# Performance work log

Measured on AMD Instinct MI355X. Metric: run time of the kernel, lower is better.

## Reference

```python
import jax, jax.numpy as jnp
import numpy as np

B, S, D_MODEL, FILTER, K, MAX_FRAMES = 16, 512, 512, 512, 3, 2048


def _conv1d(x, w, b):
    # x: [B, C, L], w: [O, I, K], padding=1 -> same length
    y = jax.lax.conv_general_dilated(x, w, window_strides=(1,), padding=[(1, 1)],
                                     dimension_numbers=("NCH", "OIH", "NCH"))
    return y + b[None, :, None]


def _predictor(x, w1, b1, w2, b2, wl, bl):
    # x: [B, L, d] -> scalar track [B, L]
    h = x.transpose(0, 2, 1)                      # [B, d, L]
    h = jax.nn.relu(_conv1d(h, w1, b1))
    h = jax.nn.relu(_conv1d(h, w2, b2))
    h = h.transpose(0, 2, 1)                      # [B, L, filter]
    return (jnp.einsum("blf,f->bl", h, wl[:, 0]) + bl[0])


def _expand_hidden(H, D, max_T):
    # Length regulator: cumsum + searchsorted gather (vectorized repeat_interleave).
    D = jnp.maximum(D, 0).astype(jnp.int32)
    csum = jnp.cumsum(D, axis=1)                  # [B, S]
    t = jnp.arange(max_T, dtype=jnp.int32)        # [T]
    # idx[b, t] = # of cumsum entries <= t  == source token index for frame t
    idx = jax.vmap(lambda c: jnp.searchsorted(c, t, side="right"))(csum)  # [B, T]
    total = csum[:, -1]                           # [B]
    valid = t[None, :] < jnp.minimum(total, max_T)[:, None]               # [B, T]
    idx_safe = jnp.minimum(idx, S - 1)
    He = jnp.take_along_axis(H, idx_safe[:, :, None], axis=1)             # [B, T, d]
    return jnp.where(valid[:, :, None], He, jnp.zeros((), He.dtype))


def setup_inputs() -> dict:
    key = jax.random.key(0)
    ks = jax.random.split(key, 24)
    def w(k, shape, scale=0.05):
        return jax.random.normal(k, shape, dtype=jnp.float32) * scale
    inp = {
        "H": jax.random.normal(ks[0], (B, S, D_MODEL), dtype=jnp.float32),
        "D_gt": jax.random.randint(ks[1], (B, S), 0, 12, dtype=jnp.int32),
        "P_gt": jax.random.normal(ks[2], (B, MAX_FRAMES), dtype=jnp.float32),
        "E_gt": jax.random.normal(ks[3], (B, MAX_FRAMES), dtype=jnp.float32),
    }
    for i, p in enumerate(["dp", "pp", "ep"]):
        kk = jax.random.split(ks[4 + i], 3)
        inp[p + "_w1"] = w(kk[0], (FILTER, D_MODEL, K))
        inp[p + "_b1"] = jnp.zeros((FILTER,), jnp.float32)
        inp[p + "_w2"] = w(kk[1], (FILTER, FILTER, K))
        inp[p + "_b2"] = jnp.zeros((FILTER,), jnp.float32)
        inp[p + "_wl"] = w(kk[2], (FILTER, 1))
        inp[p + "_bl"] = jnp.zeros((1,), jnp.float32)
    inp["pitch_w"] = w(ks[8], (D_MODEL,))
    inp["pitch_b"] = jnp.zeros((D_MODEL,), jnp.float32)
    inp["energy_w"] = w(ks[9], (D_MODEL,))
    inp["energy_b"] = jnp.zeros((D_MODEL,), jnp.float32)
    return inp


def reference(H, D_gt, P_gt, E_gt,
              dp_w1, dp_b1, dp_w2, dp_b2, dp_wl, dp_bl,
              pp_w1, pp_b1, pp_w2, pp_b2, pp_wl, pp_bl,
              ep_w1, ep_b1, ep_w2, ep_b2, ep_wl, ep_bl,
              pitch_w, pitch_b, energy_w, energy_b):
    # Training path (is_inference=False): D = D_gt, P = P_gt, E = E_gt.
    D_pred = _predictor(H, dp_w1, dp_b1, dp_w2, dp_b2, dp_wl, dp_bl)     # [B, S]
    H_exp = _expand_hidden(H, D_gt, MAX_FRAMES)                           # [B, T, d]
    P_pred = _predictor(H_exp, pp_w1, pp_b1, pp_w2, pp_b2, pp_wl, pp_bl)  # [B, T]
    E_pred = _predictor(H_exp, ep_w1, ep_b1, ep_w2, ep_b2, ep_wl, ep_bl)  # [B, T]
    P_proj = P_gt[:, :, None] * pitch_w[None, None, :] + pitch_b          # Linear(1,d)
    E_proj = E_gt[:, :, None] * energy_w[None, None, :] + energy_b
    H_adapted = H_exp + P_proj + E_proj
    return (H_adapted, D_pred, P_pred, E_pred)
```

## Files before the change

kernel.cpp:

```cpp
#include <hip/hip_runtime.h>

#define B_ 16
#define S_ 512
#define C_ 512
#define T_ 2048

typedef __attribute__((ext_vector_type(8))) short short8;
typedef __attribute__((ext_vector_type(4))) float floatx4;

__device__ __forceinline__ unsigned short f2bf(float x) {
    union { float f; unsigned u; } c; c.f = x;
    unsigned r = (c.u + 0x7fffu + ((c.u >> 16) & 1u)) >> 16;
    return (unsigned short)r;
}

__device__ __forceinline__ void gld_lds16(void* l, const void* g) {
    __builtin_amdgcn_global_load_lds(
        (const __attribute__((address_space(1))) void*)g,
        (__attribute__((address_space(3))) void*)l, 16, 0, 0);
}

__global__ void prep_kernel(const float* __restrict__ w0, const float* __restrict__ w1,
                            const float* __restrict__ w2, const float* __restrict__ w3,
                            const float* __restrict__ w4, const float* __restrict__ w5,
                            unsigned short* __restrict__ wpack,
                            const float* __restrict__ H, unsigned short* __restrict__ Hbf,
                            unsigned short* __restrict__ zrow,
                            const int* __restrict__ Dgt, int* __restrict__ ridx,
                            float* __restrict__ Dp, float* __restrict__ Pp, float* __restrict__ Ep,
                            const float* __restrict__ dbl, const float* __restrict__ pbl,
                            const float* __restrict__ ebl) {
    __shared__ int cs[S_];
    __shared__ int ps[256];
    int blk = blockIdx.x;
    int tid = threadIdx.x;
    if (blk < 6144) {
        int which = blk >> 10;
        const float* w = which == 0 ? w0 : which == 1 ? w1 : which == 2 ? w2
                       : which == 3 ? w3 : which == 4 ? w4 : w5;
        unsigned short* wp = wpack + (long)which * 786432;
        int i = (blk & 1023) * 256 + tid;
        const float* s = w + (long)i * 3;
        wp[i]          = f2bf(s[0]);
        wp[i + 262144] = f2bf(s[1]);
        wp[i + 524288] = f2bf(s[2]);
    } else if (blk < 10240) {
        int i = (blk - 6144) * 256 + tid;
        float4 v = *(const float4*)(H + (long)i * 4);
        ushort4 o;
        o.x = f2bf(v.x); o.y = f2bf(v.y); o.z = f2bf(v.z); o.w = f2bf(v.w);
        *(ushort4*)(Hbf + (long)i * 4) = o;
    } else if (blk < 10242) {
        zrow[(blk - 10240) * 256 + tid] = 0;
    } else if (blk < 10258) {
        int b = blk - 10242;
        int t2 = tid * 2;
        int d0 = Dgt[b * S_ + t2], d1 = Dgt[b * S_ + t2 + 1];
        int a0 = d0 < 0 ? 0 : d0, a1 = d1 < 0 ? 0 : d1;
        ps[tid] = a0 + a1;
        __syncthreads();
        for (int off = 1; off < 256; off <<= 1) {
            int v = (tid >= off) ? ps[tid - off] : 0;
            __syncthreads();
            ps[tid] += v;
            __syncthreads();
        }
        int incl = ps[tid];
        cs[t2] = incl - a1;
        cs[t2 + 1] = incl;
        __syncthreads();
        int total = cs[S_ - 1];
        int limit = total < T_ ? total : T_;
        for (int t = tid; t < T_; t += 256) {
            int lo = 0, hi = S_;
            while (lo < hi) { int mid = (lo + hi) >> 1; if (cs[mid] <= t) lo = mid + 1; else hi = mid; }
            if (lo > S_ - 1) lo = S_ - 1;
            ridx[b * T_ + t] = (t < limit) ? lo : -1;
        }
    } else {
        int i = (blk - 10258) * 256 + tid;
        if (i < 8192) Dp[i] = dbl[0];
        else if (i < 40960) Pp[i - 8192] = pbl[0];
        else Ep[i - 40960] = ebl[0];
    }
}

struct ConvJob {
    const unsigned short* X;
    const int* ridx;
    int Lshift;
    int Bshift;
    const unsigned short* wp;
    const float* bias;
    const float* wl;
    void* dst;
    int nxshift;
};

__global__ __launch_bounds__(256, 3) void mega_kernel(
    ConvJob j0, ConvJob j1, ConvJob j2, int e0, int e1, int e2, int mode, int aoff,
    const unsigned short* __restrict__ zrow,
    const float* __restrict__ H, const int* __restrict__ aridx,
    const float* __restrict__ Pgt, const float* __restrict__ Egt,
    const float* __restrict__ pw, const float* __restrict__ pb,
    const float* __restrict__ ew, const float* __restrict__ eb,
    float* __restrict__ aout)
{
    __shared__ unsigned short Wt[3 * 128 * 32];
    __shared__ unsigned short Xt[136 * 32 + 4096];
    const int bx = blockIdx.x;
    const int tid = threadIdx.x;

    if (bx >= e2) {
        int ab = bx - e2 + aoff;
#pragma unroll
        for (int it = 0; it < 8; ++it) {
            int i = ab * 256 + tid + it * 524288;
            int f4 = i & 127;
            int p  = i >> 7;
            int b  = p >> 11;
            int r  = aridx[p];
            float pg = Pgt[p], eg = Egt[p];
            int f = f4 << 2;
            float4 pwv = *(const float4*)(pw + f);
            float4 pbv = *(const float4*)(pb + f);
            float4 ewv = *(const float4*)(ew + f);
            float4 ebv = *(const float4*)(eb + f);
            float4 h = make_float4(0.f, 0.f, 0.f, 0.f);
            if (r >= 0) h = *(const float4*)(H + ((long)b * S_ + r) * C_ + f);
            float4 o;
            o.x = h.x + pg * pwv.x + pbv.x + eg * ewv.x + ebv.x;
            o.y = h.y + pg * pwv.y + pbv.y + eg * ewv.y + ebv.y;
            o.z = h.z + pg * pwv.z + pbv.z + eg * ewv.z + ebv.z;
            o.w = h.w + pg * pwv.w + pbv.w + eg * ewv.w + ebv.w;
            *(float4*)(aout + (long)p * C_ + f) = o;
        }
        return;
    }

    ConvJob j;
    int local;
    if (bx < e0)      { j = j0; local = bx; }
    else if (bx < e1) { j = j1; local = bx - e0; }
    else              { j = j2; local = bx - e1; }
    const int m0 = (local >> j.nxshift) * 128;
    const int n0 = (local & ((1 << j.nxshift) - 1)) * 128;
    const int L = 1 << j.Lshift;
    const int b = n0 >> j.Lshift;
    const int t0 = n0 & (L - 1);

    floatx4 acc[4][4];
#pragma unroll
    for (int i = 0; i < 4; ++i)
#pragma unroll
        for (int jj = 0; jj < 4; ++jj) acc[i][jj] = (floatx4){0.f, 0.f, 0.f, 0.f};

    const unsigned short* wptr[6];
#pragma unroll
    for (int q = 0; q < 6; ++q) {
        int idx = tid + q * 256;
        int tap = idx >> 9, rem = idx & 511;
        int row = rem >> 2;
        int sw = (rem & 3) ^ ((row >> 1) & 3);
        wptr[q] = j.wp + (long)tap * (C_ * C_) + (long)(m0 + row) * C_ + sw * 8;
    }
    auto xrow = [&](int rho) -> const unsigned short* {
        int t = t0 - 1 + rho;
        if (t < 0 || t >= L) return zrow;
        int r = j.ridx ? j.ridx[(b << j.Lshift) + t] : t;
        if (r < 0) return zrow;
        return j.X + ((long)(b << j.Bshift) + r) * C_;
    };
    const int xs = tid & 3;
    const int rho0 = tid >> 2, rho1 = 64 + (tid >> 2), rho2 = 128 + (tid >> 2);
    const unsigned short* xptr0 = xrow(rho0) + (xs ^ ((rho0 >> 1) & 3)) * 8;
    const unsigned short* xptr1 = xrow(rho1) + (xs ^ ((rho1 >> 1) & 3)) * 8;
    const unsigned short* xptr2 = (tid < 8) ? (xrow(rho2) + (xs ^ ((rho2 >> 1) & 3)) * 8) : zrow;

    char* wbase = (char*)Wt + (tid >> 6) * 1024;
    char* xbase = (char*)Xt + (tid >> 6) * 1024;

    const int lane = tid & 63;
    const int q = lane >> 4, lr = lane & 15;
    const int wm = (tid >> 6) & 1, wn = tid >> 7;
    const int qsW = (q ^ ((lr >> 1) & 3)) * 8;
    int qsX[3];
#pragma unroll
    for (int tap = 0; tap < 3; ++tap)
        qsX[tap] = (q ^ (((lr + tap) >> 1) & 3)) * 8;

    for (int c0 = 0; c0 < C_; c0 += 32) {
        __syncthreads();
#pragma unroll
        for (int qq = 0; qq < 6; ++qq)
            gld_lds16(wbase + qq * 4096, wptr[qq] + c0);
        gld_lds16(xbase, xptr0 + c0);
        gld_lds16(xbase + 4096, xptr1 + c0);
        if (tid < 8)
            gld_lds16((char*)Xt + 8192, xptr2 + c0);
        __syncthreads();
#pragma unroll
        for (int tap = 0; tap < 3; ++tap) {
            const unsigned short* Wl = Wt + ((tap * 128) + wm * 64 + lr) * 32 + qsW;
            const unsigned short* Xl = Xt + (wn * 64 + lr + tap) * 32 + qsX[tap];
            short8 a[4], bf[4];
#pragma unroll
            for (int i = 0; i < 4; ++i) {
                a[i]  = *(const short8*)(Wl + i * 16 * 32);
                bf[i] = *(const short8*)(Xl + i * 16 * 32);
            }
#pragma unroll
            for (int i = 0; i < 4; ++i)
#pragma unroll
                for (int jj = 0; jj < 4; ++jj)
                    acc[i][jj] = __builtin_amdgcn_mfma_f32_16x16x32_bf16(
                        a[i], bf[jj], acc[i][jj], 0, 0, 0);
        }
    }

    const int fbase = m0 + wm * 64 + q * 4;
    const int pbase = n0 + wn * 64 + lr;
    if (mode == 0) {
        unsigned short* dst = (unsigned short*)j.dst;
#pragma unroll
        for (int i = 0; i < 4; ++i) {
            int f = fbase + i * 16;
            float4 bv = *(const float4*)(j.bias + f);
#pragma unroll
            for (int jj = 0; jj < 4; ++jj) {
                int p = pbase + jj * 16;
                ushort4 o;
                o.x = f2bf(fmaxf(acc[i][jj][0] + bv.x, 0.f));
                o.y = f2bf(fmaxf(acc[i][jj][1] + bv.y, 0.f));
                o.z = f2bf(fmaxf(acc[i][jj][2] + bv.z, 0.f));
                o.w = f2bf(fmaxf(acc[i][jj][3] + bv.w, 0.f));
                *(ushort4*)(dst + (long)p * C_ + f) = o;
            }
        }
    } else {
        float* dst = (float*)j.dst;
#pragma unroll
        for (int jj = 0; jj < 4; ++jj) {
            float s = 0.f;
#pragma unroll
            for (int i = 0; i < 4; ++i) {
                int f = fbase + i * 16;
                float4 bv = *(const float4*)(j.bias + f);
                float4 wv = *(const float4*)(j.wl + f);
                s += fmaxf(acc[i][jj][0] + bv.x, 0.f) * wv.x;
                s += fmaxf(acc[i][jj][1] + bv.y, 0.f) * wv.y;
                s += fmaxf(acc[i][jj][2] + bv.z, 0.f) * wv.z;
                s += fmaxf(acc[i][jj][3] + bv.w, 0.f) * wv.w;
            }
            s += __shfl_xor(s, 16, 64);
            s += __shfl_xor(s, 32, 64);
            if (lane < 16) atomicAdd(dst + pbase + jj * 16, s);
        }
    }
}

extern "C" void kernel_launch(void* const* d_in, const int* in_sizes, int n_in,
                              void* d_out, int out_size, void* d_ws, size_t ws_size,
                              hipStream_t stream) {
    const float* H    = (const float*)d_in[0];
    const int*   Dgt  = (const int*)d_in[1];
    const float* Pgt  = (const float*)d_in[2];
    const float* Egt  = (const float*)d_in[3];
    const float* dp_w1 = (const float*)d_in[4];
    const float* dp_b1 = (const float*)d_in[5];
    const float* dp_w2 = (const float*)d_in[6];
    const float* dp_b2 = (const float*)d_in[7];
    const float* dp_wl = (const float*)d_in[8];
    const float* dp_bl = (const float*)d_in[9];
    const float* pp_w1 = (const float*)d_in[10];
    const float* pp_b1 = (const float*)d_in[11];
    const float* pp_w2 = (const float*)d_in[12];
    const float* pp_b2 = (const float*)d_in[13];
    const float* pp_wl = (const float*)d_in[14];
    const float* pp_bl = (const float*)d_in[15];
    const float* ep_w1 = (const float*)d_in[16];
    const float* ep_b1 = (const float*)d_in[17];
    const float* ep_w2 = (const float*)d_in[18];
    const float* ep_b2 = (const float*)d_in[19];
    const float* ep_wl = (const float*)d_in[20];
    const float* ep_bl = (const float*)d_in[21];
    const float* pitch_w  = (const float*)d_in[22];
    const float* pitch_b  = (const float*)d_in[23];
    const float* energy_w = (const float*)d_in[24];
    const float* energy_b = (const float*)d_in[25];

    float* out     = (float*)d_out;
    float* H_adapt = out;
    float* D_pred  = out + 16777216;
    float* P_pred  = out + 16785408;
    float* E_pred  = out + 16818176;

    const bool par = ws_size >= 94000000ull;

    char* ws = (char*)d_ws;
    size_t off = 0;
    unsigned short* wpack = (unsigned short*)(ws + off); off += 6UL * 786432UL * 2UL;
    unsigned short* Hbf   = (unsigned short*)(ws + off); off += 4194304UL * 2UL;
    unsigned short* h1a   = (unsigned short*)(ws + off); off += 16777216UL * 2UL;
    unsigned short* h1b   = par ? (unsigned short*)(ws + off) : h1a;
    if (par) off += 16777216UL * 2UL;
    unsigned short* h1dp  = (unsigned short*)(ws + off); off += 4194304UL * 2UL;
    unsigned short* zrow  = (unsigned short*)(ws + off); off += 512UL * 2UL;
    off = (off + 255) & ~(size_t)255;
    int* ridx_exp = (int*)(ws + off); off += (size_t)B_ * T_ * 4;

    hipLaunchKernelGGL(prep_kernel, dim3(10546), dim3(256), 0, stream,
                       dp_w1, dp_w2, pp_w1, pp_w2, ep_w1, ep_w2, wpack, H, Hbf, zrow,
                       Dgt, ridx_exp, D_pred, P_pred, E_pred, dp_bl, pp_bl, ep_bl);

    ConvJob j_pp1 = { Hbf,  ridx_exp, 11,  9, wpack + 2UL * 786432, pp_b1, nullptr, h1a,    8 };
    ConvJob j_ep1 = { Hbf,  ridx_exp, 11,  9, wpack + 4UL * 786432, ep_b1, nullptr, h1b,    8 };
    ConvJob j_dp1 = { Hbf,  nullptr,   9,  9, wpack + 0UL * 786432, dp_b1, nullptr, h1dp,   6 };
    ConvJob j_pp2 = { h1a,  nullptr,  11, 11, wpack + 3UL * 786432, pp_b2, pp_wl,  P_pred, 8 };
    ConvJob j_ep2 = { h1b,  nullptr,  11, 11, wpack + 5UL * 786432, ep_b2, ep_wl,  E_pred, 8 };
    ConvJob j_dp2 = { h1dp, nullptr,   9,  9, wpack + 1UL * 786432, dp_b2, dp_wl,  D_pred, 6 };

    if (par) {
        hipLaunchKernelGGL(mega_kernel, dim3(2304 + 1024), dim3(256), 0, stream,
                           j_pp1, j_ep1, j_dp1, 1024, 2048, 2304, 0, 0, zrow,
                           H, ridx_exp, Pgt, Egt, pitch_w, pitch_b, energy_w, energy_b, H_adapt);
        hipLaunchKernelGGL(mega_kernel, dim3(2304 + 1024), dim3(256), 0, stream,
                           j_pp2, j_ep2, j_dp2, 1024, 2048, 2304, 1, 1024, zrow,
                           H, ridx_exp, Pgt, Egt, pitch_w, pitch_b, energy_w, energy_b, H_adapt);
    } else {
        hipLaunchKernelGGL(mega_kernel, dim3(1280 + 2048), dim3(256), 0, stream,
                           j_pp1, j_dp1, j_dp1, 1024, 1280, 1280, 0, 0, zrow,
                           H, ridx_exp, Pgt, Egt, pitch_w, pitch_b, energy_w, energy_b, H_adapt);
        hipLaunchKernelGGL(mega_kernel, dim3(1280), dim3(256), 0, stream,
                           j_pp2, j_dp2, j_dp2, 1024, 1280, 1280, 1, 0, zrow,
                           H, ridx_exp, Pgt, Egt, pitch_w, pitch_b, energy_w, energy_b, H_adapt);
        hipLaunchKernelGGL(mega_kernel, dim3(1024), dim3(256), 0, stream,
                           j_ep1, j_ep1, j_ep1, 1024, 1024, 1024, 0, 0, zrow,
                           H, ridx_exp, Pgt, Egt, pitch_w, pitch_b, energy_w, energy_b, H_adapt);
        hipLaunchKernelGGL(mega_kernel, dim3(1024), dim3(256), 0, stream,
                           j_ep2, j_ep2, j_ep2, 1024, 1024, 1024, 1, 0, zrow,
                           H, ridx_exp, Pgt, Egt, pitch_w, pitch_b, energy_w, energy_b, H_adapt);
    }
}
```

Baseline: 359.4 us.

## Use 256x256 tiles with 8 waves and double-buffered LDS pipelined conv GEMM

The conv GEMM tile grows from 128x128 to 256x256, with 512-thread blocks, a 64-wide K chunk and 130KB of dynamic LDS. Weight and activation tiles are double-buffered, and the global-to-LDS loads for the next tap or chunk are interleaved between MFMA phases, using s_setprio and explicit vmcnt waits. The goal is to raise arithmetic intensity and hide load latency behind MFMA work. In exchange the grid is much smaller (576 conv blocks on about 256 CUs), so tail effects may appear, and the large LDS footprint limits occupancy to one block per CU.

New measurement: 515.1 us. 43.3% more time.

```diff
diff --git a/kernel.cpp b/kernel.cpp
--- a/kernel.cpp
+++ b/kernel.cpp
@@ -97,7 +97,53 @@
     int nxshift;
 };
 
-__global__ __launch_bounds__(256, 3) void mega_kernel(
+template <int TAP, typename F0, typename F1, typename F2, typename F3>
+__device__ __forceinline__ void kt_body(
+    floatx4 (&acc)[8][4],
+    const unsigned short* __restrict__ Wb_, const unsigned short* __restrict__ Xb_,
+    int wm, int wn, int q, int lr, F0 s0, F1 s1, F2 s2, F3 s3)
+{
+    short8 bfr[4][2];
+#pragma unroll
+    for (int jj = 0; jj < 4; ++jj) {
+        const int xr = wn * 64 + jj * 16 + lr + TAP;
+        const unsigned short* xp = Xb_ + xr * 64;
+        const int sX = xr & 7;
+        bfr[jj][0] = *(const short8*)(xp + ((q ^ sX) * 8));
+        bfr[jj][1] = *(const short8*)(xp + (((4 + q) ^ sX) * 8));
+    }
+#pragma unroll
+    for (int ph = 0; ph < 4; ++ph) {
+        const int wr = wm * 128 + ph * 32 + lr;
+        const unsigned short* ap0 = Wb_ + wr * 64;
+        const unsigned short* ap1 = ap0 + 1024;
+        const int sA = lr & 7;
+        short8 a00 = *(const short8*)(ap0 + ((q ^ sA) * 8));
+        short8 a01 = *(const short8*)(ap0 + (((4 + q) ^ sA) * 8));
+        short8 a10 = *(const short8*)(ap1 + ((q ^ sA) * 8));
+        short8 a11 = *(const short8*)(ap1 + (((4 + q) ^ sA) * 8));
+        if (ph == 0) s0(); else if (ph == 1) s1(); else if (ph == 2) s2(); else s3();
+        __builtin_amdgcn_s_setprio(1);
+#pragma unroll
+        for (int jj = 0; jj < 4; ++jj) {
+            acc[ph*2][jj]   = __builtin_amdgcn_mfma_f32_16x16x32_bf16(a00, bfr[jj][0], acc[ph*2][jj],   0, 0, 0);
+            acc[ph*2][jj]   = __builtin_amdgcn_mfma_f32_16x16x32_bf16(a01, bfr[jj][1], acc[ph*2][jj],   0, 0, 0);
+            acc[ph*2+1][jj] = __builtin_amdgcn_mfma_f32_16x16x32_bf16(a10, bfr[jj][0], acc[ph*2+1][jj], 0, 0, 0);
+            acc[ph*2+1][jj] = __builtin_amdgcn_mfma_f32_16x16x32_bf16(a11, bfr[jj][1], acc[ph*2+1][jj], 0, 0, 0);
+        }
+        __builtin_amdgcn_s_setprio(0);
+        __builtin_amdgcn_s_barrier();
+    }
+}
+
+#define VMWAIT(n) do { \
+    asm volatile("s_waitcnt vmcnt(" #n ")" ::: "memory"); \
+    __builtin_amdgcn_sched_barrier(0); \
+    __builtin_amdgcn_s_barrier(); \
+    __builtin_amdgcn_sched_barrier(0); \
+} while (0)
+
+__global__ __launch_bounds__(512, 2) void mega_kernel(
     ConvJob j0, ConvJob j1, ConvJob j2, int e0, int e1, int e2, int mode, int aoff,
     const unsigned short* __restrict__ zrow,
     const float* __restrict__ H, const int* __restrict__ aridx,
@@ -106,8 +152,7 @@
     const float* __restrict__ ew, const float* __restrict__ eb,
     float* __restrict__ aout)
 {
-    __shared__ unsigned short Wt[3 * 128 * 32];
-    __shared__ unsigned short Xt[136 * 32 + 4096];
+    extern __shared__ unsigned short lds[];
     const int bx = blockIdx.x;
     const int tid = threadIdx.x;
 
@@ -115,7 +160,7 @@
         int ab = bx - e2 + aoff;
 #pragma unroll
         for (int it = 0; it < 8; ++it) {
-            int i = ab * 256 + tid + it * 524288;
+            int i = ab * 512 + tid + it * 524288;
             int f4 = i & 127;
             int p  = i >> 7;
             int b  = p >> 11;
@@ -143,87 +188,100 @@
     if (bx < e0)      { j = j0; local = bx; }
     else if (bx < e1) { j = j1; local = bx - e0; }
     else              { j = j2; local = bx - e1; }
-    const int m0 = (local >> j.nxshift) * 128;
-    const int n0 = (local & ((1 << j.nxshift) - 1)) * 128;
+    const int m0 = (local >> j.nxshift) * 256;
+    const int n0 = (local & ((1 << j.nxshift) - 1)) * 256;
     const int L = 1 << j.Lshift;
     const int b = n0 >> j.Lshift;
     const int t0 = n0 & (L - 1);
 
-    floatx4 acc[4][4];
-#pragma unroll
-    for (int i = 0; i < 4; ++i)
+    unsigned short* WtS = lds;
+    unsigned short* XtS = lds + 32768;
+    char* WtB = (char*)WtS;
+    char* XtB = (char*)XtS;
+
+    const int w = tid >> 6, l = tid & 63;
+    const int q = l >> 4, lr = l & 15;
+    const int wm = w & 1, wn = w >> 1;
+
+    floatx4 acc[8][4];
+#pragma unroll
+    for (int i = 0; i < 8; ++i)
 #pragma unroll
         for (int jj = 0; jj < 4; ++jj) acc[i][jj] = (floatx4){0.f, 0.f, 0.f, 0.f};
 
-    const unsigned short* wptr[6];
-#pragma unroll
-    for (int q = 0; q < 6; ++q) {
-        int idx = tid + q * 256;
-        int tap = idx >> 9, rem = idx & 511;
-        int row = rem >> 2;
-        int sw = (rem & 3) ^ ((row >> 1) & 3);
-        wptr[q] = j.wp + (long)tap * (C_ * C_) + (long)(m0 + row) * C_ + sw * 8;
-    }
-    auto xrow = [&](int rho) -> const unsigned short* {
-        int t = t0 - 1 + rho;
+    const int swz = ((l & 7) ^ ((l >> 3) & 7)) * 8;
+    auto xrowp = [&](int r) -> const unsigned short* {
+        int t = t0 - 1 + r;
         if (t < 0 || t >= L) return zrow;
-        int r = j.ridx ? j.ridx[(b << j.Lshift) + t] : t;
-        if (r < 0) return zrow;
-        return j.X + ((long)(b << j.Bshift) + r) * C_;
+        int rr = j.ridx ? j.ridx[(b << j.Lshift) + t] : t;
+        if (rr < 0) return zrow;
+        return j.X + ((long)(b << j.Bshift) + rr) * C_;
     };
-    const int xs = tid & 3;
-    const int rho0 = tid >> 2, rho1 = 64 + (tid >> 2), rho2 = 128 + (tid >> 2);
-    const unsigned short* xptr0 = xrow(rho0) + (xs ^ ((rho0 >> 1) & 3)) * 8;
-    const unsigned short* xptr1 = xrow(rho1) + (xs ^ ((rho1 >> 1) & 3)) * 8;
-    const unsigned short* xptr2 = (tid < 8) ? (xrow(rho2) + (xs ^ ((rho2 >> 1) & 3)) * 8) : zrow;
-
-    char* wbase = (char*)Wt + (tid >> 6) * 1024;
-    char* xbase = (char*)Xt + (tid >> 6) * 1024;
-
-    const int lane = tid & 63;
-    const int q = lane >> 4, lr = lane & 15;
-    const int wm = (tid >> 6) & 1, wn = tid >> 7;
-    const int qsW = (q ^ ((lr >> 1) & 3)) * 8;
-    int qsX[3];
-#pragma unroll
-    for (int tap = 0; tap < 3; ++tap)
-        qsX[tap] = (q ^ (((lr + tap) >> 1) & 3)) * 8;
-
-    for (int c0 = 0; c0 < C_; c0 += 32) {
-        __syncthreads();
-#pragma unroll
-        for (int qq = 0; qq < 6; ++qq)
-            gld_lds16(wbase + qq * 4096, wptr[qq] + c0);
-        gld_lds16(xbase, xptr0 + c0);
-        gld_lds16(xbase + 4096, xptr1 + c0);
-        if (tid < 8)
-            gld_lds16((char*)Xt + 8192, xptr2 + c0);
-        __syncthreads();
-#pragma unroll
-        for (int tap = 0; tap < 3; ++tap) {
-            const unsigned short* Wl = Wt + ((tap * 128) + wm * 64 + lr) * 32 + qsW;
-            const unsigned short* Xl = Xt + (wn * 64 + lr + tap) * 32 + qsX[tap];
-            short8 a[4], bf[4];
-#pragma unroll
-            for (int i = 0; i < 4; ++i) {
-                a[i]  = *(const short8*)(Wl + i * 16 * 32);
-                bf[i] = *(const short8*)(Xl + i * 16 * 32);
-            }
-#pragma unroll
-            for (int i = 0; i < 4; ++i)
-#pragma unroll
-                for (int jj = 0; jj < 4; ++jj)
-                    acc[i][jj] = __builtin_amdgcn_mfma_f32_16x16x32_bf16(
-                        a[i], bf[jj], acc[i][jj], 0, 0, 0);
-        }
-    }
-
-    const int fbase = m0 + wm * 64 + q * 4;
+    const unsigned short* wsrc[4];
+    const unsigned short* xsrc[4];
+#pragma unroll
+    for (int qq = 0; qq < 4; ++qq) {
+        int row = qq * 64 + w * 8 + (l >> 3);
+        wsrc[qq] = j.wp + (long)(m0 + row) * C_ + swz;
+        xsrc[qq] = xrowp(row) + swz;
+    }
+    const int ch_e = w * 2 + (l & 1);
+    const int row_e = 256 + (ch_e >> 3);
+    const unsigned short* xsrcE = xrowp(row_e) + (((ch_e & 7) ^ (row_e & 7)) * 8);
+
+    auto issueW = [&](int buf, int qq, int koff) {
+        gld_lds16(WtB + buf * 32768 + qq * 8192 + w * 1024, wsrc[qq] + koff);
+    };
+    auto issueX = [&](int buf, int qq, int xoff) {
+        gld_lds16(XtB + buf * 33024 + qq * 8192 + w * 1024, xsrc[qq] + xoff);
+    };
+    auto issueXe = [&](int buf, int xoff) {
+        if (l < 2) gld_lds16(XtB + buf * 33024 + 32768 + w * 32, xsrcE + xoff);
+    };
+
+    issueX(0, 0, 0); issueX(0, 1, 0); issueX(0, 2, 0); issueX(0, 3, 0); issueXe(0, 0);
+    issueW(0, 0, 0); issueW(0, 1, 0); issueW(0, 2, 0); issueW(0, 3, 0);
+
+#pragma unroll 1
+    for (int cc = 0; cc < 8; ++cc) {
+        const int xb = cc & 1;
+        const int wb0 = cc & 1, wb1 = wb0 ^ 1;
+        const unsigned short* Xb = XtS + xb * 16512;
+        const int kW1 = 262144 + cc * 64;
+        const int kW2 = 524288 + cc * 64;
+        const int kW0n = cc * 64 + 64;
+        const int xoffn = cc * 64 + 64;
+        const bool more = (cc < 7);
+
+        VMWAIT(0);
+        kt_body<0>(acc, WtS + wb0 * 16384, Xb, wm, wn, q, lr,
+            [&]{ issueW(wb1, 0, kW1); },
+            [&]{ issueW(wb1, 1, kW1); },
+            [&]{ issueW(wb1, 2, kW1); issueW(wb1, 3, kW1); },
+            [&]{});
+
+        VMWAIT(0);
+        kt_body<1>(acc, WtS + wb1 * 16384, Xb, wm, wn, q, lr,
+            [&]{ issueW(wb0, 0, kW2); issueW(wb0, 1, kW2); },
+            [&]{ issueW(wb0, 2, kW2); issueW(wb0, 3, kW2); },
+            [&]{ if (more) { issueX(xb ^ 1, 0, xoffn); issueX(xb ^ 1, 1, xoffn);
+                             issueX(xb ^ 1, 2, xoffn); issueX(xb ^ 1, 3, xoffn); } },
+            [&]{ if (more) issueXe(xb ^ 1, xoffn); });
+
+        if (more) { VMWAIT(5); } else { VMWAIT(0); }
+        kt_body<2>(acc, WtS + wb0 * 16384, Xb, wm, wn, q, lr,
+            [&]{ if (more) issueW(wb1, 0, kW0n); },
+            [&]{ if (more) issueW(wb1, 1, kW0n); },
+            [&]{ if (more) { issueW(wb1, 2, kW0n); issueW(wb1, 3, kW0n); } },
+            [&]{});
+    }
+
+    const int fbase = m0 + wm * 128 + q * 4;
     const int pbase = n0 + wn * 64 + lr;
     if (mode == 0) {
         unsigned short* dst = (unsigned short*)j.dst;
 #pragma unroll
-        for (int i = 0; i < 4; ++i) {
+        for (int i = 0; i < 8; ++i) {
             int f = fbase + i * 16;
             float4 bv = *(const float4*)(j.bias + f);
 #pragma unroll
@@ -243,7 +301,7 @@
         for (int jj = 0; jj < 4; ++jj) {
             float s = 0.f;
 #pragma unroll
-            for (int i = 0; i < 4; ++i) {
+            for (int i = 0; i < 8; ++i) {
                 int f = fbase + i * 16;
                 float4 bv = *(const float4*)(j.bias + f);
                 float4 wv = *(const float4*)(j.wl + f);
@@ -254,7 +312,7 @@
             }
             s += __shfl_xor(s, 16, 64);
             s += __shfl_xor(s, 32, 64);
-            if (lane < 16) atomicAdd(dst + pbase + jj * 16, s);
+            if (l < 16) atomicAdd(dst + pbase + jj * 16, s);
         }
     }
 }
@@ -313,32 +371,34 @@
                        dp_w1, dp_w2, pp_w1, pp_w2, ep_w1, ep_w2, wpack, H, Hbf, zrow,
                        Dgt, ridx_exp, D_pred, P_pred, E_pred, dp_bl, pp_bl, ep_bl);
 
-    ConvJob j_pp1 = { Hbf,  ridx_exp, 11,  9, wpack + 2UL * 786432, pp_b1, nullptr, h1a,    8 };
-    ConvJob j_ep1 = { Hbf,  ridx_exp, 11,  9, wpack + 4UL * 786432, ep_b1, nullptr, h1b,    8 };
-    ConvJob j_dp1 = { Hbf,  nullptr,   9,  9, wpack + 0UL * 786432, dp_b1, nullptr, h1dp,   6 };
-    ConvJob j_pp2 = { h1a,  nullptr,  11, 11, wpack + 3UL * 786432, pp_b2, pp_wl,  P_pred, 8 };
-    ConvJob j_ep2 = { h1b,  nullptr,  11, 11, wpack + 5UL * 786432, ep_b2, ep_wl,  E_pred, 8 };
-    ConvJob j_dp2 = { h1dp, nullptr,   9,  9, wpack + 1UL * 786432, dp_b2, dp_wl,  D_pred, 6 };
+    ConvJob j_pp1 = { Hbf,  ridx_exp, 11,  9, wpack + 2UL * 786432, pp_b1, nullptr, h1a,    7 };
+    ConvJob j_ep1 = { Hbf,  ridx_exp, 11,  9, wpack + 4UL * 786432, ep_b1, nullptr, h1b,    7 };
+    ConvJob j_dp1 = { Hbf,  nullptr,   9,  9, wpack + 0UL * 786432, dp_b1, nullptr, h1dp,   5 };
+    ConvJob j_pp2 = { h1a,  nullptr,  11, 11, wpack + 3UL * 786432, pp_b2, pp_wl,  P_pred, 7 };
+    ConvJob j_ep2 = { h1b,  nullptr,  11, 11, wpack + 5UL * 786432, ep_b2, ep_wl,  E_pred, 7 };
+    ConvJob j_dp2 = { h1dp, nullptr,   9,  9, wpack + 1UL * 786432, dp_b2, dp_wl,  D_pred, 5 };
+
+    const unsigned lds_bytes = 131584;
 
     if (par) {
-        hipLaunchKernelGGL(mega_kernel, dim3(2304 + 1024), dim3(256), 0, stream,
-                           j_pp1, j_ep1, j_dp1, 1024, 2048, 2304, 0, 0, zrow,
-                           H, ridx_exp, Pgt, Egt, pitch_w, pitch_b, energy_w, energy_b, H_adapt);
-        hipLaunchKernelGGL(mega_kernel, dim3(2304 + 1024), dim3(256), 0, stream,
-                           j_pp2, j_ep2, j_dp2, 1024, 2048, 2304, 1, 1024, zrow,
+        hipLaunchKernelGGL(mega_kernel, dim3(576 + 512), dim3(512), lds_bytes, stream,
+                           j_pp1, j_ep1, j_dp1, 256, 512, 576, 0, 0, zrow,
+                           H, ridx_exp, Pgt, Egt, pitch_w, pitch_b, energy_w, energy_b, H_adapt);
+        hipLaunchKernelGGL(mega_kernel, dim3(576 + 512), dim3(512), lds_bytes, stream,
+                           j_pp2, j_ep2, j_dp2, 256, 512, 576, 1, 512, zrow,
                            H, ridx_exp, Pgt, Egt, pitch_w, pitch_b, energy_w, energy_b, H_adapt);
     } else {
-        hipLaunchKernelGGL(mega_kernel, dim3(1280 + 2048), dim3(256), 0, stream,
-                           j_pp1, j_dp1, j_dp1, 1024, 1280, 1280, 0, 0, zrow,
-                           H, ridx_exp, Pgt, Egt, pitch_w, pitch_b, energy_w, energy_b, H_adapt);
-        hipLaunchKernelGGL(mega_kernel, dim3(1280), dim3(256), 0, stream,
-                           j_pp2, j_dp2, j_dp2, 1024, 1280, 1280, 1, 0, zrow,
-                           H, ridx_exp, Pgt, Egt, pitch_w, pitch_b, energy_w, energy_b, H_adapt);
-        hipLaunchKernelGGL(mega_kernel, dim3(1024), dim3(256), 0, stream,
-                           j_ep1, j_ep1, j_ep1, 1024, 1024, 1024, 0, 0, zrow,
-                           H, ridx_exp, Pgt, Egt, pitch_w, pitch_b, energy_w, energy_b, H_adapt);
-        hipLaunchKernelGGL(mega_kernel, dim3(1024), dim3(256), 0, stream,
-                           j_ep2, j_ep2, j_ep2, 1024, 1024, 1024, 1, 0, zrow,
-                           H, ridx_exp, Pgt, Egt, pitch_w, pitch_b, energy_w, energy_b, H_adapt);
-    }
-}
+        hipLaunchKernelGGL(mega_kernel, dim3(320 + 1024), dim3(512), lds_bytes, stream,
+                           j_pp1, j_dp1, j_dp1, 256, 320, 320, 0, 0, zrow,
+                           H, ridx_exp, Pgt, Egt, pitch_w, pitch_b, energy_w, energy_b, H_adapt);
+        hipLaunchKernelGGL(mega_kernel, dim3(320), dim3(512), lds_bytes, stream,
+                           j_pp2, j_dp2, j_dp2, 256, 320, 320, 1, 0, zrow,
+                           H, ridx_exp, Pgt, Egt, pitch_w, pitch_b, energy_w, energy_b, H_adapt);
+        hipLaunchKernelGGL(mega_kernel, dim3(256), dim3(512), lds_bytes, stream,
+                           j_ep1, j_ep1, j_ep1, 256, 256, 256, 0, 0, zrow,
+                           H, ridx_exp, Pgt, Egt, pitch_w, pitch_b, energy_w, energy_b, H_adapt);
+        hipLaunchKernelGGL(mega_kernel, dim3(256), dim3(512), lds_bytes, stream,
+                           j_ep2, j_ep2, j_ep2, 256, 256, 256, 1, 0, zrow,
+                           H, ridx_exp, Pgt, Egt, pitch_w, pitch_b, energy_w, energy_b, H_adapt);
+    }
+}
```

## Double-buffer per-tap weight and input tiles to overlap loads with MFMA

Applied to the files above, without the earlier changes.

Restructures the conv GEMM main loop so weight tiles are loaded one tap at a time into two alternating LDS buffers, and input tiles into two buffers. The load for the next tap or chunk is issued before the current tap's MFMAs run, with explicit vmcnt waits and barriers. Before, all three taps were loaded and then computed with a full sync in between. Shared memory moves to dynamic allocation of about 33 KB and occupancy hint rises to 4 blocks per CU. This hides global-to-LDS latency but adds more barriers per chunk and relies on hand-tuned wait counts that must match the number of loads in flight.

New measurement: 352.9 us. No clear change (-1.8%).

```diff
diff --git a/kernel.cpp b/kernel.cpp
--- a/kernel.cpp
+++ b/kernel.cpp
@@ -97,7 +97,38 @@
     int nxshift;
 };
 
-__global__ __launch_bounds__(256, 3) void mega_kernel(
+template <int TAP>
+__device__ __forceinline__ void compute_kt(
+    floatx4 (&acc)[4][4],
+    const unsigned short* Wb, const unsigned short* Xb,
+    int wm, int wn, int q, int lr)
+{
+    short8 bfr[4];
+    const int sX = ((lr + TAP) >> 1) & 3;
+#pragma unroll
+    for (int jj = 0; jj < 4; ++jj) {
+        const int xr = wn * 64 + jj * 16 + lr + TAP;
+        bfr[jj] = *(const short8*)(Xb + xr * 32 + ((q ^ sX) * 8));
+    }
+    const int sA = (lr >> 1) & 3;
+#pragma unroll
+    for (int i = 0; i < 4; ++i) {
+        const int rA = wm * 64 + i * 16 + lr;
+        short8 a = *(const short8*)(Wb + rA * 32 + ((q ^ sA) * 8));
+#pragma unroll
+        for (int jj = 0; jj < 4; ++jj)
+            acc[i][jj] = __builtin_amdgcn_mfma_f32_16x16x32_bf16(a, bfr[jj], acc[i][jj], 0, 0, 0);
+    }
+}
+
+#define VMWAIT(n) do { \
+    asm volatile("s_waitcnt vmcnt(" #n ")" ::: "memory"); \
+    __builtin_amdgcn_sched_barrier(0); \
+    __builtin_amdgcn_s_barrier(); \
+    __builtin_amdgcn_sched_barrier(0); \
+} while (0)
+
+__global__ __launch_bounds__(256, 4) void mega_kernel(
     ConvJob j0, ConvJob j1, ConvJob j2, int e0, int e1, int e2, int mode, int aoff,
     const unsigned short* __restrict__ zrow,
     const float* __restrict__ H, const int* __restrict__ aridx,
@@ -106,8 +137,7 @@
     const float* __restrict__ ew, const float* __restrict__ eb,
     float* __restrict__ aout)
 {
-    __shared__ unsigned short Wt[3 * 128 * 32];
-    __shared__ unsigned short Xt[136 * 32 + 4096];
+    extern __shared__ unsigned short lds[];
     const int bx = blockIdx.x;
     const int tid = threadIdx.x;
 
@@ -149,73 +179,78 @@
     const int b = n0 >> j.Lshift;
     const int t0 = n0 & (L - 1);
 
+    unsigned short* WtS = lds;
+    unsigned short* XtS = lds + 8192;
+    char* WtB = (char*)WtS;
+    char* XtB = (char*)XtS;
+
+    const int w = tid >> 6, l = tid & 63;
+    const int q = l >> 4, lr = l & 15;
+    const int wm = w & 1, wn = w >> 1;
+
     floatx4 acc[4][4];
 #pragma unroll
     for (int i = 0; i < 4; ++i)
 #pragma unroll
         for (int jj = 0; jj < 4; ++jj) acc[i][jj] = (floatx4){0.f, 0.f, 0.f, 0.f};
 
-    const unsigned short* wptr[6];
-#pragma unroll
-    for (int q = 0; q < 6; ++q) {
-        int idx = tid + q * 256;
-        int tap = idx >> 9, rem = idx & 511;
-        int row = rem >> 2;
-        int sw = (rem & 3) ^ ((row >> 1) & 3);
-        wptr[q] = j.wp + (long)tap * (C_ * C_) + (long)(m0 + row) * C_ + sw * 8;
-    }
-    auto xrow = [&](int rho) -> const unsigned short* {
-        int t = t0 - 1 + rho;
+    const int sw = (((tid & 3) ^ ((tid >> 3) & 3))) * 8;
+    auto xrowp = [&](int r) -> const unsigned short* {
+        int t = t0 - 1 + r;
         if (t < 0 || t >= L) return zrow;
-        int r = j.ridx ? j.ridx[(b << j.Lshift) + t] : t;
-        if (r < 0) return zrow;
-        return j.X + ((long)(b << j.Bshift) + r) * C_;
+        int rr = j.ridx ? j.ridx[(b << j.Lshift) + t] : t;
+        if (rr < 0) return zrow;
+        return j.X + ((long)(b << j.Bshift) + rr) * C_;
     };
-    const int xs = tid & 3;
-    const int rho0 = tid >> 2, rho1 = 64 + (tid >> 2), rho2 = 128 + (tid >> 2);
-    const unsigned short* xptr0 = xrow(rho0) + (xs ^ ((rho0 >> 1) & 3)) * 8;
-    const unsigned short* xptr1 = xrow(rho1) + (xs ^ ((rho1 >> 1) & 3)) * 8;
-    const unsigned short* xptr2 = (tid < 8) ? (xrow(rho2) + (xs ^ ((rho2 >> 1) & 3)) * 8) : zrow;
-
-    char* wbase = (char*)Wt + (tid >> 6) * 1024;
-    char* xbase = (char*)Xt + (tid >> 6) * 1024;
-
-    const int lane = tid & 63;
-    const int q = lane >> 4, lr = lane & 15;
-    const int wm = (tid >> 6) & 1, wn = tid >> 7;
-    const int qsW = (q ^ ((lr >> 1) & 3)) * 8;
-    int qsX[3];
-#pragma unroll
-    for (int tap = 0; tap < 3; ++tap)
-        qsX[tap] = (q ^ (((lr + tap) >> 1) & 3)) * 8;
-
-    for (int c0 = 0; c0 < C_; c0 += 32) {
-        __syncthreads();
-#pragma unroll
-        for (int qq = 0; qq < 6; ++qq)
-            gld_lds16(wbase + qq * 4096, wptr[qq] + c0);
-        gld_lds16(xbase, xptr0 + c0);
-        gld_lds16(xbase + 4096, xptr1 + c0);
-        if (tid < 8)
-            gld_lds16((char*)Xt + 8192, xptr2 + c0);
-        __syncthreads();
-#pragma unroll
-        for (int tap = 0; tap < 3; ++tap) {
-            const unsigned short* Wl = Wt + ((tap * 128) + wm * 64 + lr) * 32 + qsW;
-            const unsigned short* Xl = Xt + (wn * 64 + lr + tap) * 32 + qsX[tap];
-            short8 a[4], bf[4];
-#pragma unroll
-            for (int i = 0; i < 4; ++i) {
-                a[i]  = *(const short8*)(Wl + i * 16 * 32);
-                bf[i] = *(const short8*)(Xl + i * 16 * 32);
-            }
-#pragma unroll
-            for (int i = 0; i < 4; ++i)
-#pragma unroll
-                for (int jj = 0; jj < 4; ++jj)
-                    acc[i][jj] = __builtin_amdgcn_mfma_f32_16x16x32_bf16(
-                        a[i], bf[jj], acc[i][jj], 0, 0, 0);
-        }
+    const unsigned short* wsrc[2];
+    const unsigned short* xsrc[2];
+#pragma unroll
+    for (int qq = 0; qq < 2; ++qq) {
+        int row = qq * 64 + (tid >> 2);
+        wsrc[qq] = j.wp + (long)(m0 + row) * C_ + sw;
+        xsrc[qq] = xrowp(row) + sw;
+    }
+    const int ch_e = w * 2 + (l & 1);
+    const unsigned short* xsrcE = xrowp(128 + (ch_e >> 2)) + (ch_e & 3) * 8;
+
+    auto issueW = [&](int buf, int koff) {
+        gld_lds16(WtB + buf * 8192 + 0 * 4096 + w * 1024, wsrc[0] + koff);
+        gld_lds16(WtB + buf * 8192 + 1 * 4096 + w * 1024, wsrc[1] + koff);
+    };
+    auto issueX = [&](int buf, int xoff) {
+        gld_lds16(XtB + buf * 8320 + 0 * 4096 + w * 1024, xsrc[0] + xoff);
+        gld_lds16(XtB + buf * 8320 + 1 * 4096 + w * 1024, xsrc[1] + xoff);
+        if (l < 2)
+            gld_lds16(XtB + buf * 8320 + 8192 + w * 32, xsrcE + xoff);
+    };
+
+    issueX(0, 0);
+    issueW(0, 0);
+
+#pragma unroll 1
+    for (int cc = 0; cc < 16; ++cc) {
+        const int xb = cc & 1;
+        const unsigned short* Xb = XtS + xb * 4160;
+        const unsigned short* W0 = WtS + xb * 4096;
+        const unsigned short* W1 = WtS + (xb ^ 1) * 4096;
+        const int kW1 = 262144 + cc * 32;
+        const int kW2 = 524288 + cc * 32;
+        const int kW0n = cc * 32 + 32;
+        const int xoffn = cc * 32 + 32;
+        const bool more = (cc < 15);
+
+        VMWAIT(0);
+        issueW(xb ^ 1, kW1);
+        compute_kt<0>(acc, W0, Xb, wm, wn, q, lr);
+
+        VMWAIT(0);
+        issueW(xb, kW2);
+        if (more) issueX(xb ^ 1, xoffn);
+        compute_kt<1>(acc, W1, Xb, wm, wn, q, lr);
+
+        if (more) { VMWAIT(3); } else { VMWAIT(0); }
+        if (more) issueW(xb ^ 1, kW0n);
+        compute_kt<2>(acc, W0, Xb, wm, wn, q, lr);
     }
 
     const int fbase = m0 + wm * 64 + q * 4;
@@ -254,7 +289,7 @@
             }
             s += __shfl_xor(s, 16, 64);
             s += __shfl_xor(s, 32, 64);
-            if (lane < 16) atomicAdd(dst + pbase + jj * 16, s);
+            if (l < 16) atomicAdd(dst + pbase + jj * 16, s);
         }
     }
 }
@@ -320,24 +355,26 @@
     ConvJob j_ep2 = { h1b,  nullptr,  11, 11, wpack + 5UL * 786432, ep_b2, ep_wl,  E_pred, 8 };
     ConvJob j_dp2 = { h1dp, nullptr,   9,  9, wpack + 1UL * 786432, dp_b2, dp_wl,  D_pred, 6 };
 
+    const unsigned lds_bytes = 33024;
+
     if (par) {
-        hipLaunchKernelGGL(mega_kernel, dim3(2304 + 1024), dim3(256), 0, stream,
+        hipLaunchKernelGGL(mega_kernel, dim3(2304 + 1024), dim3(256), lds_bytes, stream,
                            j_pp1, j_ep1, j_dp1, 1024, 2048, 2304, 0, 0, zrow,
                            H, ridx_exp, Pgt, Egt, pitch_w, pitch_b, energy_w, energy_b, H_adapt);
-        hipLaunchKernelGGL(mega_kernel, dim3(2304 + 1024), dim3(256), 0, stream,
+        hipLaunchKernelGGL(mega_kernel, dim3(2304 + 1024), dim3(256), lds_bytes, stream,
                            j_pp2, j_ep2, j_dp2, 1024, 2048, 2304, 1, 1024, zrow,
                            H, ridx_exp, Pgt, Egt, pitch_w, pitch_b, energy_w, energy_b, H_adapt);
     } else {
-        hipLaunchKernelGGL(mega_kernel, dim3(1280 + 2048), dim3(256), 0, stream,
+        hipLaunchKernelGGL(mega_kernel, dim3(1280 + 2048), dim3(256), lds_bytes, stream,
                            j_pp1, j_dp1, j_dp1, 1024, 1280, 1280, 0, 0, zrow,
                            H, ridx_exp, Pgt, Egt, pitch_w, pitch_b, energy_w, energy_b, H_adapt);
-        hipLaunchKernelGGL(mega_kernel, dim3(1280), dim3(256), 0, stream,
+        hipLaunchKernelGGL(mega_kernel, dim3(1280), dim3(256), lds_bytes, stream,
                            j_pp2, j_dp2, j_dp2, 1024, 1280, 1280, 1, 0, zrow,
                            H, ridx_exp, Pgt, Egt, pitch_w, pitch_b, energy_w, energy_b, H_adapt);
-        hipLaunchKernelGGL(mega_kernel, dim3(1024), dim3(256), 0, stream,
+        hipLaunchKernelGGL(mega_kernel, dim3(1024), dim3(256), lds_bytes, stream,
                            j_ep1, j_ep1, j_ep1, 1024, 1024, 1024, 0, 0, zrow,
                            H, ridx_exp, Pgt, Egt, pitch_w, pitch_b, energy_w, energy_b, H_adapt);
-        hipLaunchKernelGGL(mega_kernel, dim3(1024), dim3(256), 0, stream,
+        hipLaunchKernelGGL(mega_kernel, dim3(1024), dim3(256), lds_bytes, stream,
                            j_ep2, j_ep2, j_ep2, 1024, 1024, 1024, 1, 0, zrow,
                            H, ridx_exp, Pgt, Egt, pitch_w, pitch_b, energy_w, energy_b, H_adapt);
     }
```
